# Kernel tuning notes

Hardware: AMD Instinct MI355X
Metric: run time of the kernel (lower is better)

Reference implementation:

```python
import jax, jax.numpy as jnp
import numpy as np


def setup_inputs() -> dict:
    key = jax.random.key(0)
    k1, k2, k3 = jax.random.split(key, 3)
    B, C, H, W = 4, 3, 1024, 1920
    im0 = jax.random.normal(k1, (B, C, H, W), dtype=jnp.float32)
    # realistic optical-flow displacements of a few pixels
    flow = jax.random.normal(k2, (B, H, W, 2), dtype=jnp.float32) * 5.0
    flowback = jax.random.normal(k3, (B, H, W, 2), dtype=jnp.float32) * 5.0
    return {"im0": im0, "flow": flow, "flowback": flowback, "interpolation_mode": 0}


def _splat(im0, flow, interpolation_mode):
    # im0: [B,C,H,W], flow: [B,H,W,2] (dx, dy)
    B, C, H, W = im0.shape
    src = jnp.transpose(im0, (0, 2, 3, 1)).reshape(B * H * W, C)  # [BHW, C]
    gy, gx = jnp.meshgrid(jnp.arange(H, dtype=jnp.float32),
                          jnp.arange(W, dtype=jnp.float32), indexing="ij")
    x = gx[None] + flow[..., 0]  # [B,H,W] target x coord
    y = gy[None] + flow[..., 1]  # [B,H,W] target y coord
    b_idx = jnp.arange(B, dtype=jnp.int32)[:, None, None] * (H * W)  # batch offset

    out_flat = jnp.zeros((B * H * W, C), dtype=im0.dtype)

    if interpolation_mode == 1:  # Nearest
        xi = jnp.round(x).astype(jnp.int32)
        yi = jnp.round(y).astype(jnp.int32)
        corners = [(xi, yi, jnp.ones_like(x))]
    else:  # Bilinear: scatter-add to 4 neighbors
        x0 = jnp.floor(x).astype(jnp.int32)
        y0 = jnp.floor(y).astype(jnp.int32)
        x1, y1 = x0 + 1, y0 + 1
        x0f, y0f = x0.astype(x.dtype), y0.astype(y.dtype)
        wx1, wy1 = x - x0f, y - y0f
        wx0, wy0 = 1.0 - wx1, 1.0 - wy1
        corners = [(x0, y0, wx0 * wy0), (x1, y0, wx1 * wy0),
                   (x0, y1, wx0 * wy1), (x1, y1, wx1 * wy1)]

    for xi, yi, wgt in corners:
        valid = (xi >= 0) & (xi < W) & (yi >= 0) & (yi < H)
        w = wgt * valid.astype(im0.dtype)
        xc = jnp.clip(xi, 0, W - 1)
        yc = jnp.clip(yi, 0, H - 1)
        idx = (b_idx + yc * W + xc).reshape(-1)  # [BHW]
        out_flat = out_flat.at[idx].add(src * w.reshape(-1, 1))

    return jnp.transpose(out_flat.reshape(B, H, W, C), (0, 3, 1, 2))


def reference(im0, flow, flowback, interpolation_mode):
    # flowback is accepted (as in the CUDA extension signature) but the
    # forward splat itself only consumes im0 and the forward flow.
    return _splat(im0, flow, interpolation_mode)
```

## Files before the change

kernel.cpp:

```cpp
#include <hip/hip_runtime.h>

constexpr int B_ = 4;
constexpr int C_ = 3;
constexpr int H_ = 1024;
constexpr int W_ = 1920;
constexpr int HW_ = H_ * W_;

constexpr int TW = 128;
constexpr int TH = 64;
constexpr int R  = 16;
constexpr int EW = TW + 2 * R;
constexpr int EH = TH + 2 * R;
constexpr int ECELLS = EW * EH;

static_assert(W_ % TW == 0 && H_ % TH == 0, "exact tiling assumed");

__global__ __launch_bounds__(256) void forward_warp_tiled(
    const float* __restrict__ im0,
    const float2* __restrict__ flow,
    const int* __restrict__ mode_p,
    float* __restrict__ out) {
    __shared__ float tile[ECELLS];

    const int tx0 = blockIdx.x * TW;
    const int ty0 = blockIdx.y * TH;
    const int b   = blockIdx.z;
    const int mode = *mode_p;
    const int ex0 = tx0 - R;
    const int ey0 = ty0 - R;

    for (int c = 0; c < C_; ++c) {
        for (int i = threadIdx.x; i < ECELLS; i += 256) tile[i] = 0.0f;
        __syncthreads();

        const float* im0c = im0 + ((size_t)(b * C_ + c)) * HW_;
        float* outc = out + ((size_t)(b * C_ + c)) * HW_;

        for (int p = threadIdx.x; p < TW * TH; p += 256) {
            const int lx = p & (TW - 1);
            const int ly = p >> 7;
            const int x = tx0 + lx;
            const int y = ty0 + ly;
            const float2 f = flow[(size_t)(b * H_ + y) * W_ + x];
            const float s = im0c[y * W_ + x];
            const float px = (float)x + f.x;
            const float py = (float)y + f.y;

            int   cx[4], cy[4];
            float cw[4];
            int ncorn;
            if (mode == 1) {
                cx[0] = (int)rintf(px);
                cy[0] = (int)rintf(py);
                cw[0] = 1.0f;
                ncorn = 1;
            } else {
                const float xf = floorf(px), yf = floorf(py);
                const int x0 = (int)xf, y0i = (int)yf;
                const float wx1 = px - xf, wy1 = py - yf;
                const float wx0 = 1.0f - wx1, wy0 = 1.0f - wy1;
                cx[0] = x0;     cy[0] = y0i;     cw[0] = wx0 * wy0;
                cx[1] = x0 + 1; cy[1] = y0i;     cw[1] = wx1 * wy0;
                cx[2] = x0;     cy[2] = y0i + 1; cw[2] = wx0 * wy1;
                cx[3] = x0 + 1; cy[3] = y0i + 1; cw[3] = wx1 * wy1;
                ncorn = 4;
            }
            for (int k = 0; k < ncorn; ++k) {
                const int exi = cx[k] - ex0;
                const int eyi = cy[k] - ey0;
                const float v = s * cw[k];
                if ((unsigned)exi < (unsigned)EW && (unsigned)eyi < (unsigned)EH) {
                    atomicAdd(&tile[eyi * EW + exi], v);
                } else if ((unsigned)cx[k] < (unsigned)W_ &&
                           (unsigned)cy[k] < (unsigned)H_) {
                    unsafeAtomicAdd(outc + cy[k] * W_ + cx[k], v);
                }
            }
        }
        __syncthreads();

        for (int i = threadIdx.x; i < ECELLS; i += 256) {
            const float v = tile[i];
            if (v != 0.0f) {
                const int exi = i % EW;
                const int eyi = i / EW;
                const int gx = ex0 + exi;
                const int gy = ey0 + eyi;
                if ((unsigned)gx < (unsigned)W_ && (unsigned)gy < (unsigned)H_)
                    unsafeAtomicAdd(outc + gy * W_ + gx, v);
            }
        }
        __syncthreads();
    }
}

extern "C" void kernel_launch(void* const* d_in, const int* in_sizes, int n_in,
                              void* d_out, int out_size, void* d_ws, size_t ws_size,
                              hipStream_t stream) {
    const float*  im0  = (const float*)d_in[0];
    const float2* flow = (const float2*)d_in[1];
    const int*    mode = (const int*)d_in[3];
    float* out = (float*)d_out;

    (void)hipMemsetAsync(d_out, 0, (size_t)out_size * sizeof(float), stream);

    dim3 grid(W_ / TW, H_ / TH, B_);
    forward_warp_tiled<<<grid, dim3(256), 0, stream>>>(im0, flow, mode, out);
}
```

Before: 733.3 us.

## Replace tile scatter with destination-owned gather plus separate far-flow pass

Each block now owns one output tile. It scans a source halo of radius R, accumulates every contribution landing inside its tile in shared memory for all three channels, and writes the tile with plain float4 stores. This removes the global memset and almost all global atomics. A second grid-stride kernel handles only contributions displaced more than R, using global atomics; those are rare for flows of a few pixels. The cost is that halo flow reads are redundant (about 2.25x), and correctness depends on the near/far split being exact.

```diff
diff --git a/kernel.cpp b/kernel.cpp
--- a/kernel.cpp
+++ b/kernel.cpp
@@ -6,91 +6,184 @@
 constexpr int W_ = 1920;
 constexpr int HW_ = H_ * W_;
 
-constexpr int TW = 128;
+constexpr int TW = 64;
 constexpr int TH = 64;
 constexpr int R  = 16;
 constexpr int EW = TW + 2 * R;
 constexpr int EH = TH + 2 * R;
-constexpr int ECELLS = EW * EH;
+constexpr int TCELLS = TW * TH;
+constexpr int NTHR = 512;
 
 static_assert(W_ % TW == 0 && H_ % TH == 0, "exact tiling assumed");
 
-__global__ __launch_bounds__(256) void forward_warp_tiled(
+__global__ __launch_bounds__(NTHR, 6) void fw_gather(
     const float* __restrict__ im0,
     const float2* __restrict__ flow,
     const int* __restrict__ mode_p,
     float* __restrict__ out) {
-    __shared__ float tile[ECELLS];
+    __shared__ float tile[C_][TCELLS];
 
     const int tx0 = blockIdx.x * TW;
     const int ty0 = blockIdx.y * TH;
     const int b   = blockIdx.z;
     const int mode = *mode_p;
-    const int ex0 = tx0 - R;
-    const int ey0 = ty0 - R;
-
-    for (int c = 0; c < C_; ++c) {
-        for (int i = threadIdx.x; i < ECELLS; i += 256) tile[i] = 0.0f;
-        __syncthreads();
-
-        const float* im0c = im0 + ((size_t)(b * C_ + c)) * HW_;
-        float* outc = out + ((size_t)(b * C_ + c)) * HW_;
-
-        for (int p = threadIdx.x; p < TW * TH; p += 256) {
-            const int lx = p & (TW - 1);
-            const int ly = p >> 7;
-            const int x = tx0 + lx;
-            const int y = ty0 + ly;
-            const float2 f = flow[(size_t)(b * H_ + y) * W_ + x];
-            const float s = im0c[y * W_ + x];
-            const float px = (float)x + f.x;
-            const float py = (float)y + f.y;
-
-            int   cx[4], cy[4];
-            float cw[4];
-            int ncorn;
-            if (mode == 1) {
-                cx[0] = (int)rintf(px);
-                cy[0] = (int)rintf(py);
-                cw[0] = 1.0f;
-                ncorn = 1;
-            } else {
-                const float xf = floorf(px), yf = floorf(py);
-                const int x0 = (int)xf, y0i = (int)yf;
-                const float wx1 = px - xf, wy1 = py - yf;
-                const float wx0 = 1.0f - wx1, wy0 = 1.0f - wy1;
-                cx[0] = x0;     cy[0] = y0i;     cw[0] = wx0 * wy0;
-                cx[1] = x0 + 1; cy[1] = y0i;     cw[1] = wx1 * wy0;
-                cx[2] = x0;     cy[2] = y0i + 1; cw[2] = wx0 * wy1;
-                cx[3] = x0 + 1; cy[3] = y0i + 1; cw[3] = wx1 * wy1;
-                ncorn = 4;
-            }
-            for (int k = 0; k < ncorn; ++k) {
-                const int exi = cx[k] - ex0;
-                const int eyi = cy[k] - ey0;
-                const float v = s * cw[k];
-                if ((unsigned)exi < (unsigned)EW && (unsigned)eyi < (unsigned)EH) {
-                    atomicAdd(&tile[eyi * EW + exi], v);
-                } else if ((unsigned)cx[k] < (unsigned)W_ &&
-                           (unsigned)cy[k] < (unsigned)H_) {
-                    unsafeAtomicAdd(outc + cy[k] * W_ + cx[k], v);
+
+    float* t0 = &tile[0][0];
+    for (int i = threadIdx.x; i < C_ * TCELLS; i += NTHR) t0[i] = 0.0f;
+    __syncthreads();
+
+    const float*  im0b  = im0  + (size_t)b * C_ * HW_;
+    const float2* flowb = flow + (size_t)b * HW_;
+
+    for (int p = threadIdx.x; p < EW * EH; p += NTHR) {
+        const int ly = p / EW;
+        const int lx = p - ly * EW;
+        const int gx = tx0 - R + lx;
+        const int gy = ty0 - R + ly;
+        if ((unsigned)gx >= (unsigned)W_ || (unsigned)gy >= (unsigned)H_)
+            continue;
+
+        const float2 f = flowb[gy * W_ + gx];
+        const float px = (float)gx + f.x;
+        const float py = (float)gy + f.y;
+
+        if (mode == 1) {
+            const int cx = (int)rintf(px);
+            const int cy = (int)rintf(py);
+            const int ltx = cx - tx0, lty = cy - ty0;
+            const int dx = cx - gx, dy = cy - gy;
+            if ((unsigned)ltx < (unsigned)TW && (unsigned)lty < (unsigned)TH &&
+                dx >= -R && dx <= R && dy >= -R && dy <= R) {
+                const int src = gy * W_ + gx;
+                const int idx = lty * TW + ltx;
+                atomicAdd(&tile[0][idx], im0b[src]);
+                atomicAdd(&tile[1][idx], im0b[src + HW_]);
+                atomicAdd(&tile[2][idx], im0b[src + 2 * HW_]);
+            }
+        } else {
+            const float xf = floorf(px), yf = floorf(py);
+            const int x0 = (int)xf, y0 = (int)yf;
+            const float wx1 = px - xf, wy1 = py - yf;
+            const float wx0 = 1.0f - wx1, wy0 = 1.0f - wy1;
+
+            const int   cxs[4] = { x0, x0 + 1, x0,     x0 + 1 };
+            const int   cys[4] = { y0, y0,     y0 + 1, y0 + 1 };
+            const float cws[4] = { wx0 * wy0, wx1 * wy0, wx0 * wy1, wx1 * wy1 };
+
+            bool m[4];
+            bool any = false;
+#pragma unroll
+            for (int k = 0; k < 4; ++k) {
+                const int ltx = cxs[k] - tx0, lty = cys[k] - ty0;
+                const int dx = cxs[k] - gx, dy = cys[k] - gy;
+                m[k] = ((unsigned)ltx < (unsigned)TW) &&
+                       ((unsigned)lty < (unsigned)TH) &&
+                       (dx >= -R) && (dx <= R) && (dy >= -R) && (dy <= R);
+                any = any || m[k];
+            }
+            if (!any) continue;
+
+            const int src = gy * W_ + gx;
+            const float s0 = im0b[src];
+            const float s1 = im0b[src + HW_];
+            const float s2 = im0b[src + 2 * HW_];
+#pragma unroll
+            for (int k = 0; k < 4; ++k) {
+                if (m[k]) {
+                    const int idx = (cys[k] - ty0) * TW + (cxs[k] - tx0);
+                    const float w = cws[k];
+                    atomicAdd(&tile[0][idx], s0 * w);
+                    atomicAdd(&tile[1][idx], s1 * w);
+                    atomicAdd(&tile[2][idx], s2 * w);
                 }
             }
         }
-        __syncthreads();
-
-        for (int i = threadIdx.x; i < ECELLS; i += 256) {
-            const float v = tile[i];
-            if (v != 0.0f) {
-                const int exi = i % EW;
-                const int eyi = i / EW;
-                const int gx = ex0 + exi;
-                const int gy = ey0 + eyi;
-                if ((unsigned)gx < (unsigned)W_ && (unsigned)gy < (unsigned)H_)
-                    unsafeAtomicAdd(outc + gy * W_ + gx, v);
+    }
+    __syncthreads();
+
+    for (int i = threadIdx.x; i < C_ * (TCELLS / 4); i += NTHR) {
+        const int c    = i >> 10;
+        const int j    = i & 1023;
+        const int row  = j >> 4;
+        const int col4 = j & 15;
+        const float4 v = reinterpret_cast<const float4*>(&tile[c][0])[j];
+        float* dst = out + ((size_t)(b * C_ + c)) * HW_ +
+                     (size_t)(ty0 + row) * W_ + tx0 + col4 * 4;
+        *reinterpret_cast<float4*>(dst) = v;
+    }
+}
+
+__global__ __launch_bounds__(256) void fw_far(
+    const float* __restrict__ im0,
+    const float2* __restrict__ flow,
+    const int* __restrict__ mode_p,
+    float* __restrict__ out) {
+    const int mode = *mode_p;
+    const int total = B_ * HW_;
+    const float lim = (float)(R - 1);
+    for (int idx = blockIdx.x * 256 + threadIdx.x; idx < total;
+         idx += gridDim.x * 256) {
+        const float2 f = flow[idx];
+        if (fabsf(f.x) < lim && fabsf(f.y) < lim) continue;
+
+        const int b   = idx / HW_;
+        const int rem = idx - b * HW_;
+        const int gy  = rem / W_;
+        const int gx  = rem - gy * W_;
+        const float px = (float)gx + f.x;
+        const float py = (float)gy + f.y;
+        const float* im0b = im0 + (size_t)b * C_ * HW_;
+        float*       outb = out + (size_t)b * C_ * HW_;
+        const int src = gy * W_ + gx;
+
+        if (mode == 1) {
+            const int cx = (int)rintf(px);
+            const int cy = (int)rintf(py);
+            const int dx = cx - gx, dy = cy - gy;
+            const bool in = (unsigned)cx < (unsigned)W_ &&
+                            (unsigned)cy < (unsigned)H_;
+            if (in && (dx < -R || dx > R || dy < -R || dy > R)) {
+                const int dsti = cy * W_ + cx;
+                unsafeAtomicAdd(outb + dsti,            im0b[src]);
+                unsafeAtomicAdd(outb + HW_ + dsti,      im0b[src + HW_]);
+                unsafeAtomicAdd(outb + 2 * HW_ + dsti,  im0b[src + 2 * HW_]);
+            }
+        } else {
+            const float xf = floorf(px), yf = floorf(py);
+            const int x0 = (int)xf, y0 = (int)yf;
+            const float wx1 = px - xf, wy1 = py - yf;
+            const float wx0 = 1.0f - wx1, wy0 = 1.0f - wy1;
+
+            const int   cxs[4] = { x0, x0 + 1, x0,     x0 + 1 };
+            const int   cys[4] = { y0, y0,     y0 + 1, y0 + 1 };
+            const float cws[4] = { wx0 * wy0, wx1 * wy0, wx0 * wy1, wx1 * wy1 };
+
+            bool m[4];
+            bool any = false;
+#pragma unroll
+            for (int k = 0; k < 4; ++k) {
+                const int dx = cxs[k] - gx, dy = cys[k] - gy;
+                const bool in = (unsigned)cxs[k] < (unsigned)W_ &&
+                                (unsigned)cys[k] < (unsigned)H_;
+                m[k] = in && (dx < -R || dx > R || dy < -R || dy > R);
+                any = any || m[k];
+            }
+            if (!any) continue;
+
+            const float s0 = im0b[src];
+            const float s1 = im0b[src + HW_];
+            const float s2 = im0b[src + 2 * HW_];
+#pragma unroll
+            for (int k = 0; k < 4; ++k) {
+                if (m[k]) {
+                    const int dsti = cys[k] * W_ + cxs[k];
+                    const float w = cws[k];
+                    unsafeAtomicAdd(outb + dsti,           s0 * w);
+                    unsafeAtomicAdd(outb + HW_ + dsti,     s1 * w);
+                    unsafeAtomicAdd(outb + 2 * HW_ + dsti, s2 * w);
+                }
             }
         }
-        __syncthreads();
     }
 }
 
@@ -102,8 +195,7 @@
     const int*    mode = (const int*)d_in[3];
     float* out = (float*)d_out;
 
-    (void)hipMemsetAsync(d_out, 0, (size_t)out_size * sizeof(float), stream);
-
     dim3 grid(W_ / TW, H_ / TH, B_);
-    forward_warp_tiled<<<grid, dim3(256), 0, stream>>>(im0, flow, mode, out);
+    fw_gather<<<grid, dim3(NTHR), 0, stream>>>(im0, flow, mode, out);
+    fw_far<<<dim3(2048), dim3(256), 0, stream>>>(im0, flow, mode, out);
 }
```

New measurement: 699.2 us. -4.6%, faster.
